# Performance work log

Measured on AMD Instinct MI355X. Metric: run time of the kernel, lower is better.

The kernel has to match this reference:

```python
import jax, jax.numpy as jnp
import numpy as np

B, N, C = 2, 2048, 768
H, HD = 12, 64
HID = 3072
LN_EPS = 1e-5
POL_EPS = 1e-6


def _layer_norm(x, g, b):
    m = jnp.mean(x, axis=-1, keepdims=True)
    v = jnp.mean(jnp.square(x - m), axis=-1, keepdims=True)
    return (x - m) * jax.lax.rsqrt(v + LN_EPS) * g + b


def _softmax_with_policy(attn, policy):
    # attn: [B,H,N,N], policy: [B,N,1]
    n = attn.shape[-1]
    ap = policy.reshape(policy.shape[0], 1, 1, n)  # [B,1,1,N]
    eye = jnp.eye(n, dtype=ap.dtype)[None, None]   # [1,1,N,N]
    ap = ap + (1.0 - ap) * eye                     # always attend to self
    attn = attn - jnp.max(attn, axis=-1, keepdims=True)
    attn = jnp.exp(attn.astype(jnp.float32)) * ap.astype(jnp.float32)
    attn = (attn + POL_EPS / n) / (jnp.sum(attn, axis=-1, keepdims=True) + POL_EPS)
    return attn


def setup_inputs() -> dict:
    key = jax.random.key(0)
    ks = jax.random.split(key, 12)
    s = lambda fan_in: 1.0 / np.sqrt(fan_in)
    x = jax.random.normal(ks[0], (B, N, C), dtype=jnp.float32)
    policy = (jax.random.uniform(ks[1], (B, N, 1)) > 0.5).astype(jnp.float32)
    return {
        "x": x,
        "policy": policy,
        "ln1_g": jnp.ones((C,), jnp.float32),
        "ln1_b": jnp.zeros((C,), jnp.float32),
        "qkv_w": jax.random.uniform(ks[2], (3 * H * HD, C), jnp.float32, -s(C), s(C)),
        "proj_w": jax.random.uniform(ks[3], (C, H * HD), jnp.float32, -s(H * HD), s(H * HD)),
        "proj_b": jnp.zeros((C,), jnp.float32),
        "ln2_g": jnp.ones((C,), jnp.float32),
        "ln2_b": jnp.zeros((C,), jnp.float32),
        "fc1_w": jax.random.uniform(ks[4], (HID, C), jnp.float32, -s(C), s(C)),
        "fc1_b": jnp.zeros((HID,), jnp.float32),
        "fc2_w": jax.random.uniform(ks[5], (C, HID), jnp.float32, -s(HID), s(HID)),
        "fc2_b": jnp.zeros((C,), jnp.float32),
    }


def reference(x, policy, ln1_g, ln1_b, qkv_w, proj_w, proj_b, ln2_g, ln2_b, fc1_w, fc1_b, fc2_w, fc2_b):
    b, n, c = x.shape
    scale = HD ** -0.5
    # --- attention branch (pre-LN) ---
    h = _layer_norm(x, ln1_g, ln1_b)
    qkv = (h @ qkv_w.T).reshape(b, n, 3, H, HD).transpose(2, 0, 3, 1, 4)  # [3,B,H,N,hd]
    q, k, v = qkv[0], qkv[1], qkv[2]
    attn = jnp.einsum("bhqd,bhkd->bhqk", q * scale, k)
    attn = _softmax_with_policy(attn, policy).astype(x.dtype)
    o = jnp.einsum("bhqk,bhkd->bhqd", attn, v).transpose(0, 2, 1, 3).reshape(b, n, H * HD)
    x = x + (o @ proj_w.T + proj_b)  # skip_lam = 1.0, dropout/drop_path = identity
    # --- MLP branch (pre-LN) ---
    h = _layer_norm(x, ln2_g, ln2_b)
    h = jax.nn.gelu(h @ fc1_w.T + fc1_b, approximate=False)  # torch nn.GELU = exact erf
    x = x + (h @ fc2_w.T + fc2_b)
    return x
```

## Files before the change

kernel.cpp:

```cpp
#include <hip/hip_runtime.h>

typedef unsigned short u16;
typedef unsigned int u32;
typedef float f32x4 __attribute__((ext_vector_type(4)));
typedef float f32x16 __attribute__((ext_vector_type(16)));
typedef __bf16 bf16x8 __attribute__((ext_vector_type(8)));
typedef u16 u16x4v __attribute__((ext_vector_type(4)));
typedef u32 u32x2 __attribute__((ext_vector_type(2)));
typedef u32 u32x4 __attribute__((ext_vector_type(4)));

#define NHEAD 12
#define NN 2048
#define CC 768

#define GLOBAL_AS __attribute__((address_space(1)))
#define LDS_AS __attribute__((address_space(3)))

__device__ __forceinline__ u16 tobf(float f) {
  __bf16 h = (__bf16)f;
  return __builtin_bit_cast(u16, h);
}
__device__ __forceinline__ float bf2f(u16 h) {
  u32 u = ((u32)h) << 16;
  return __builtin_bit_cast(float, u);
}
__device__ __forceinline__ u32 cvtpk(float lo, float hi) {
  u32 r;
  asm("v_cvt_pk_bf16_f32 %0, %1, %2" : "=v"(r) : "v"(lo), "v"(hi));
  return r;
}
__device__ __forceinline__ void plswap(u32& a, u32& b) {
  asm volatile("v_permlane32_swap_b32 %0, %1" : "+v"(a), "+v"(b));
}
__device__ __forceinline__ void plswapf(float& a, float& b) {
  asm volatile("v_permlane32_swap_b32 %0, %1" : "+v"(a), "+v"(b));
}
__device__ __forceinline__ float gelu_erf(float v) {
  float y = fabsf(v) * 0.70710678118654752f;
  float t = __builtin_amdgcn_rcpf(fmaf(0.3275911f, y, 1.f));
  float p = fmaf(1.061405429f, t, -1.453152027f);
  p = fmaf(p, t, 1.421413741f);
  p = fmaf(p, t, -0.284496736f);
  p = fmaf(p, t, 0.254829592f);
  p = p * t;
  float e = __builtin_amdgcn_exp2f(-y * y * 1.44269504f);
  float er = fmaf(-p, e, 1.f);
  er = (v < 0.f) ? -er : er;
  return 0.5f * v * (1.f + er);
}

#define N4_QKV 442368
#define N4_PROJ 147456
#define N4_FC 589824
__global__ __launch_bounds__(256) void cvt4_kernel(
    const float* __restrict__ a, const float* __restrict__ b,
    const float* __restrict__ c, const float* __restrict__ d,
    u16* __restrict__ oa, u16* __restrict__ ob, u16* __restrict__ oc,
    u16* __restrict__ od) {
  int i = blockIdx.x * 256 + threadIdx.x;
  const float* src;
  u16* dst;
  if (i < N4_QKV) {
    src = a; dst = oa;
  } else if (i < N4_QKV + N4_PROJ) {
    i -= N4_QKV; src = b; dst = ob;
  } else if (i < N4_QKV + N4_PROJ + N4_FC) {
    i -= N4_QKV + N4_PROJ; src = c; dst = oc;
  } else {
    i -= N4_QKV + N4_PROJ + N4_FC; src = d; dst = od;
    if (i >= N4_FC) return;
  }
  float4 v = ((const float4*)src)[i];
  u16x4v o = {tobf(v.x), tobf(v.y), tobf(v.z), tobf(v.w)};
  ((u16x4v*)dst)[i] = o;
}

__global__ __launch_bounds__(256) void ln_kernel(const float* __restrict__ x,
                                                 const float* __restrict__ gw,
                                                 const float* __restrict__ bw,
                                                 u16* __restrict__ out) {
  int row = blockIdx.x * 4 + (threadIdx.x >> 6);
  int lane = threadIdx.x & 63;
  const float* xr = x + (size_t)row * CC + lane * 12;
  float v[12];
  *(float4*)&v[0] = *(const float4*)(xr + 0);
  *(float4*)&v[4] = *(const float4*)(xr + 4);
  *(float4*)&v[8] = *(const float4*)(xr + 8);
  float s = 0.f, sq = 0.f;
#pragma unroll
  for (int j = 0; j < 12; ++j) { s += v[j]; sq += v[j] * v[j]; }
#pragma unroll
  for (int o = 1; o < 64; o <<= 1) { s += __shfl_xor(s, o); sq += __shfl_xor(sq, o); }
  float mean = s * (1.f / CC);
  float var = sq * (1.f / CC) - mean * mean;
  float rs = rsqrtf(var + 1e-5f);
  u16 ob[12];
#pragma unroll
  for (int j = 0; j < 12; ++j) {
    int c = lane * 12 + j;
    ob[j] = tobf((v[j] - mean) * rs * gw[c] + bw[c]);
  }
  u32* orow = (u32*)(out + (size_t)row * CC + lane * 12);
#pragma unroll
  for (int j = 0; j < 6; ++j) orow[j] = (u32)ob[2 * j] | ((u32)ob[2 * j + 1] << 16);
}

template <int BM, int BN, int OB, int HASB, int ACT, int RES>
__global__ __launch_bounds__(256) void gemm_kernel(
    const u16* __restrict__ A, const u16* __restrict__ Bw,
    const float* __restrict__ bias, const float* __restrict__ res,
    void* __restrict__ Cout, int M, int N, int K) {
  constexpr int MW = BM / 2;
  constexpr int MF = MW / 16;
  constexpr int NF = BN / 32;
  __shared__ __align__(16) u16 Alds[BM * 64];
  __shared__ __align__(16) u16 Blds[BN * 64];
  const int tid = threadIdx.x;
  const int lane = tid & 63, wave = tid >> 6;
  const int l15 = lane & 15, g = lane >> 4;
  const int nx = gridDim.x;
  const int flat = blockIdx.y * nx + blockIdx.x;
  const int cpx = (nx * gridDim.y) >> 3;
  const int swz = (flat & 7) * cpx + (flat >> 3);
  const int bm = (swz % nx) * BM, bn = (swz / nx) * BN;
  const int wm = (wave >> 1) * MW, wn = (wave & 1) * (BN / 2);
  f32x4 acc[MF][NF] = {};

  for (int kt = 0; kt < K; kt += 64) {
#pragma unroll
    for (int i = 0; i < BM / 32; ++i) {
      int ob_ = i * 4096 + wave * 1024;
      int lb = ob_ + lane * 16;
      int row = lb >> 7;
      int cb = (lb & 127) ^ ((row & 7) << 4);
      const u16* sa = A + (size_t)(bm + row) * K + kt + (cb >> 1);
      __builtin_amdgcn_global_load_lds((const GLOBAL_AS void*)sa,
                                       (LDS_AS void*)(Alds + (ob_ >> 1)), 16, 0, 0);
    }
#pragma unroll
    for (int i = 0; i < BN / 32; ++i) {
      int ob_ = i * 4096 + wave * 1024;
      int lb = ob_ + lane * 16;
      int row = lb >> 7;
      int cb = (lb & 127) ^ ((row & 7) << 4);
      const u16* sb = Bw + (size_t)(bn + row) * K + kt + (cb >> 1);
      __builtin_amdgcn_global_load_lds((const GLOBAL_AS void*)sb,
                                       (LDS_AS void*)(Blds + (ob_ >> 1)), 16, 0, 0);
    }
    __syncthreads();
#pragma unroll
    for (int ks = 0; ks < 2; ++ks) {
      bf16x8 af[MF], bfr[NF];
#pragma unroll
      for (int mi = 0; mi < MF; ++mi) {
        int row = wm + mi * 16 + l15;
        int cb = (ks * 64 + g * 16) ^ ((row & 7) << 4);
        af[mi] = *(const bf16x8*)&Alds[row * 64 + (cb >> 1)];
      }
#pragma unroll
      for (int ni = 0; ni < NF; ++ni) {
        int row = wn + ni * 16 + l15;
        int cb = (ks * 64 + g * 16) ^ ((row & 7) << 4);
        bfr[ni] = *(const bf16x8*)&Blds[row * 64 + (cb >> 1)];
      }
#pragma unroll
      for (int mi = 0; mi < MF; ++mi)
#pragma unroll
        for (int ni = 0; ni < NF; ++ni)
          acc[mi][ni] = __builtin_amdgcn_mfma_f32_16x16x32_bf16(af[mi], bfr[ni],
                                                                acc[mi][ni], 0, 0, 0);
    }
    __syncthreads();
  }
#pragma unroll
  for (int mi = 0; mi < MF; ++mi) {
#pragma unroll
    for (int ni = 0; ni < NF; ++ni) {
      int col = bn + wn + ni * 16 + l15;
      float bs = HASB ? bias[col] : 0.f;
#pragma unroll
      for (int r = 0; r < 4; ++r) {
        int rowm = bm + wm + mi * 16 + g * 4 + r;
        float v = acc[mi][ni][r] + bs;
        if (ACT) v = gelu_erf(v);
        if (RES) v += res[(size_t)rowm * N + col];
        if (OB)
          ((u16*)Cout)[(size_t)rowm * N + col] = tobf(v);
        else
          ((float*)Cout)[(size_t)rowm * N + col] = v;
      }
    }
  }
}

__global__ __launch_bounds__(256) void vsum_kernel(const u16* __restrict__ qkv,
                                                   float* __restrict__ vs) {
  int bh = blockIdx.x, q4 = blockIdx.y;
  int b = bh / NHEAD, h = bh % NHEAD;
  int d = threadIdx.x & 63, part = threadIdx.x >> 6;
  float s = 0.f;
  for (int n = q4 * 512 + part; n < q4 * 512 + 512; n += 4)
    s += bf2f(qkv[(size_t)(b * NN + n) * 2304 + 2 * CC + h * 64 + d]);
  __shared__ float red[256];
  red[threadIdx.x] = s;
  __syncthreads();
  if (threadIdx.x < 64) {
    float t = red[threadIdx.x] + red[threadIdx.x + 64] + red[threadIdx.x + 128] +
              red[threadIdx.x + 192];
    vs[q4 * (24 * 64) + bh * 64 + threadIdx.x] = t;
  }
}

__global__ __launch_bounds__(256) void scan_kernel(const float* __restrict__ policy,
                                                   int* __restrict__ ncbuf,
                                                   int* __restrict__ idxbuf) {
  int b = blockIdx.x, tid = threadIdx.x;
  float pv[8];
  *(float4*)&pv[0] = *(const float4*)&policy[b * NN + tid * 8];
  *(float4*)&pv[4] = *(const float4*)&policy[b * NN + tid * 8 + 4];
  int cnt = 0;
#pragma unroll
  for (int j = 0; j < 8; ++j) cnt += (pv[j] != 0.f) ? 1 : 0;
  __shared__ int sc[256];
  sc[tid] = cnt;
  __syncthreads();
  for (int off = 1; off < 256; off <<= 1) {
    int v = sc[tid];
    int add = (tid >= off) ? sc[tid - off] : 0;
    __syncthreads();
    sc[tid] = v + add;
    __syncthreads();
  }
  int base = sc[tid] - cnt;
#pragma unroll
  for (int j = 0; j < 8; ++j) {
    if (pv[j] != 0.f) idxbuf[b * NN + base++] = tid * 8 + j;
  }
  if (tid == 255) ncbuf[b] = sc[255];
}

__global__ __launch_bounds__(256) void gather_kernel(const u16* __restrict__ qkv,
                                                     const int* __restrict__ ncbuf,
                                                     const int* __restrict__ idxbuf,
                                                     u16* __restrict__ ckv) {
  int b = blockIdx.y;
  int nc = ncbuf[b];
  int ncp = (nc + 127) & ~127;
  int c = blockIdx.x * 256 + threadIdx.x;
  int j = c / 192, col = (c % 192) * 8;
  if (j >= ncp) return;
  uint4 val = {0, 0, 0, 0};
  if (j < nc) {
    int src = idxbuf[b * NN + j];
    val = *(const uint4*)&qkv[(size_t)(b * NN + src) * 2304 + CC + col];
  }
  *(uint4*)&ckv[(size_t)(b * NN + j) * 1536 + col] = val;
}

#define SCL2E 0.18033688f
#define TRRD(dst, addr, OFF) \
  asm volatile("ds_read_b64_tr_b16 %0, %1 offset:" OFF : "=v"(dst) : "v"(addr))

__global__ __launch_bounds__(256) void attn32_kernel(const u16* __restrict__ qkv,
                                                     const u16* __restrict__ ckv,
                                                     const int* __restrict__ ncbuf,
                                                     float* __restrict__ partO,
                                                     float* __restrict__ partlm) {
  __shared__ __align__(16) u16 Klds[2][4096];
  __shared__ __align__(16) u16 Vlds[2][4096];
  __shared__ float alf[4][32];
  const int bh = blockIdx.y, b = bh / NHEAD, h = bh % NHEAD;
  const int qt = blockIdx.x >> 1, half = blockIdx.x & 1;
  const int tid = threadIdx.x, lane = tid & 63, w = tid >> 6;
  const int l31 = lane & 31, hp = lane >> 5, b4 = (lane >> 4) & 1;
  const int q0 = qt * 128 + w * 32;
  const int nc = ncbuf[b];
  const int ncp = (nc + 127) & ~127;
  const int nh = ncp >> 1;
  const int nt = nh >> 6;
  const int kv0 = half * nh;
  const size_t adv = (size_t)64 * 1536;

  bf16x8 qf0, qf1, qf2, qf3;
  {
    const u16* qp = qkv + (size_t)(b * NN + q0 + l31) * 2304 + h * 64 + 8 * hp;
#pragma unroll
    for (int ds = 0; ds < 4; ++ds) {
      bf16x8 r = *(const bf16x8*)(qp + ds * 16);
      bf16x8 o;
#pragma unroll
      for (int j = 0; j < 8; ++j) o[j] = (__bf16)((float)r[j] * SCL2E);
      if (ds == 0) qf0 = o; else if (ds == 1) qf1 = o; else if (ds == 2) qf2 = o; else qf3 = o;
    }
  }

  const u16* ksrc[2];
  const u16* vsrcp[2];
#pragma unroll
  for (int c = 0; c < 2; ++c) {
    int lb = c * 4096 + w * 1024 + lane * 16;
    int row = lb >> 7;
    int cb = (lb & 127) ^ ((row & 7) << 4);
    ksrc[c] = ckv + (size_t)(b * NN + kv0 + row) * 1536 + h * 64 + (cb >> 1);
    int idx0 = (c * 256 + w * 64 + lane) * 8;
    int s0 = idx0 & 15, jj = (idx0 >> 4) & 3, b4v = (idx0 >> 6) & 1,
        pv = (idx0 >> 7) & 1, hv = (idx0 >> 8) & 1, dtv = (idx0 >> 9) & 1,
        mkv = (idx0 >> 10) & 3;
    int key = mkv * 16 + 8 * hv + 4 * pv + jj;
    int d0 = dtv * 32 + 16 * b4v + s0;
    vsrcp[c] = ckv + (size_t)(b * NN + kv0 + key) * 1536 + CC + h * 64 + d0;
  }
  auto stage = [&](int buf) {
#pragma unroll
    for (int c = 0; c < 2; ++c) {
      __builtin_amdgcn_global_load_lds((const GLOBAL_AS void*)ksrc[c],
                                       (LDS_AS void*)&Klds[buf][c * 2048 + w * 512], 16, 0, 0);
      __builtin_amdgcn_global_load_lds((const GLOBAL_AS void*)vsrcp[c],
                                       (LDS_AS void*)&Vlds[buf][c * 2048 + w * 512], 16, 0, 0);
      ksrc[c] += adv; vsrcp[c] += adv;
    }
  };

  stage(0);
  __syncthreads();

  float m_cur = -3.0e38f, m_true = -3.0e38f, l_run = 0.f;
  f32x16 accd[2] = {};
  const u32 vbase = (u32)(uintptr_t)(LDS_AS u16*)&Vlds[0][0] +
                    (u32)(2 * (lane & 15) + 128 * b4 + 512 * hp);

#pragma unroll 1
  for (int t = 0; t < nt; ++t) {
    const int cur = t & 1;
    if (t < nt - 1) stage(cur ^ 1);

    f32x16 sv0, sv1;
    {
      bf16x8 kf[4];
#pragma unroll
      for (int ds = 0; ds < 4; ++ds) {
        int row = l31;
        int cb = (32 * ds + 16 * hp) ^ ((row & 7) << 4);
        kf[ds] = *(const bf16x8*)((const char*)&Klds[cur][0] + row * 128 + cb);
      }
      f32x16 a = {};
      a = __builtin_amdgcn_mfma_f32_32x32x16_bf16(kf[0], qf0, a, 0, 0, 0);
      a = __builtin_amdgcn_mfma_f32_32x32x16_bf16(kf[1], qf1, a, 0, 0, 0);
      a = __builtin_amdgcn_mfma_f32_32x32x16_bf16(kf[2], qf2, a, 0, 0, 0);
      a = __builtin_amdgcn_mfma_f32_32x32x16_bf16(kf[3], qf3, a, 0, 0, 0);
      sv0 = a;
    }
    {
      bf16x8 kf[4];
#pragma unroll
      for (int ds = 0; ds < 4; ++ds) {
        int row = 32 + l31;
        int cb = (32 * ds + 16 * hp) ^ ((row & 7) << 4);
        kf[ds] = *(const bf16x8*)((const char*)&Klds[cur][0] + row * 128 + cb);
      }
      f32x16 a = {};
      a = __builtin_amdgcn_mfma_f32_32x32x16_bf16(kf[0], qf0, a, 0, 0, 0);
      a = __builtin_amdgcn_mfma_f32_32x32x16_bf16(kf[1], qf1, a, 0, 0, 0);
      a = __builtin_amdgcn_mfma_f32_32x32x16_bf16(kf[2], qf2, a, 0, 0, 0);
      a = __builtin_amdgcn_mfma_f32_32x32x16_bf16(kf[3], qf3, a, 0, 0, 0);
      sv1 = a;
    }

    u32x2 tr[4][2][2];
    {
      u32 vab = vbase + (u32)(cur * 8192);
      TRRD(tr[0][0][0], vab, "0");    TRRD(tr[0][0][1], vab, "256");
      TRRD(tr[0][1][0], vab, "1024"); TRRD(tr[0][1][1], vab, "1280");
      TRRD(tr[1][0][0], vab, "2048"); TRRD(tr[1][0][1], vab, "2304");
      TRRD(tr[1][1][0], vab, "3072"); TRRD(tr[1][1][1], vab, "3328");
      TRRD(tr[2][0][0], vab, "4096"); TRRD(tr[2][0][1], vab, "4352");
      TRRD(tr[3][0][0], vab, "6144"); TRRD(tr[3][0][1], vab, "6400");
      TRRD(tr[2][1][0], vab, "5120"); TRRD(tr[2][1][1], vab, "5376");
      TRRD(tr[3][1][0], vab, "7168"); TRRD(tr[3][1][1], vab, "7424");
    }

    float ta = fmaxf(fmaxf(sv0[0], sv0[1]), sv0[2]);
    float tb = fmaxf(fmaxf(sv0[3], sv0[4]), sv0[5]);
    float tc = fmaxf(fmaxf(sv0[6], sv0[7]), sv0[8]);
    float td = fmaxf(fmaxf(sv0[9], sv0[10]), sv0[11]);
    float te = fmaxf(fmaxf(sv0[12], sv0[13]), sv0[14]);
    float tf = fmaxf(fmaxf(sv0[15], sv1[0]), sv1[1]);
    float tg = fmaxf(fmaxf(sv1[2], sv1[3]), sv1[4]);
    float th = fmaxf(fmaxf(sv1[5], sv1[6]), sv1[7]);
    float ti = fmaxf(fmaxf(sv1[8], sv1[9]), sv1[10]);
    float tj = fmaxf(fmaxf(sv1[11], sv1[12]), sv1[13]);
    float tk = fmaxf(sv1[14], sv1[15]);
    float tmax = fmaxf(fmaxf(fmaxf(fmaxf(ta, tb), fmaxf(tc, td)),
                             fmaxf(fmaxf(te, tf), fmaxf(tg, th))),
                       fmaxf(fmaxf(ti, tj), tk));
    {
      float t1 = tmax, t2 = tmax;
      plswapf(t1, t2);
      tmax = fmaxf(t1, t2);
    }
    m_true = fmaxf(m_true, tmax);
    const bool defer = __all(tmax <= m_cur + 8.f);
    const float m_new = defer ? m_cur : fmaxf(m_cur, tmax);

    const int thr = nc - (kv0 + t * 64);
    float ev[32];
#pragma unroll
    for (int kt = 0; kt < 2; ++kt) {
#pragma unroll
      for (int i = 0; i < 4; ++i) {
#pragma unroll
        for (int rq = 0; rq < 4; ++rq) {
          int r = 4 * i + rq;
          int kidx = kt * 32 + 8 * i + 4 * hp + rq;
          float sval = kt ? sv1[r] : sv0[r];
          float e = __builtin_amdgcn_exp2f(sval - m_new);
          ev[kt * 16 + r] = (kidx < thr) ? e : 0.f;
        }
      }
    }
    u32 wv[16];
#pragma unroll
    for (int j = 0; j < 16; ++j) wv[j] = cvtpk(ev[2 * j], ev[2 * j + 1]);
    float ps[16];
#pragma unroll
    for (int j = 0; j < 16; ++j)
      ps[j] = __builtin_bit_cast(float, wv[j] << 16) +
              __builtin_bit_cast(float, wv[j] & 0xffff0000u);
#pragma unroll
    for (int s = 8; s > 0; s >>= 1)
#pragma unroll
      for (int j = 0; j < s; ++j) ps[j] += ps[j + s];
    float psum = ps[0];
    {
      float s1 = psum, s2 = psum;
      plswapf(s1, s2);
      psum = s1 + s2;
    }
    if (!defer) {
      float alpha = __builtin_amdgcn_exp2f(m_cur - m_new);
      l_run = l_run * alpha + psum;
      m_cur = m_new;
      if (lane < 32) alf[w][lane] = alpha;
      float4 aq0 = *(const float4*)&alf[w][4 * hp];
      float4 aq1 = *(const float4*)&alf[w][8 + 4 * hp];
      float4 aq2 = *(const float4*)&alf[w][16 + 4 * hp];
      float4 aq3 = *(const float4*)&alf[w][24 + 4 * hp];
#pragma unroll
      for (int dt = 0; dt < 2; ++dt) {
#pragma unroll
        for (int rq = 0; rq < 4; ++rq) {
          accd[dt][0 + rq] *= ((const float*)&aq0)[rq];
          accd[dt][4 + rq] *= ((const float*)&aq1)[rq];
          accd[dt][8 + rq] *= ((const float*)&aq2)[rq];
          accd[dt][12 + rq] *= ((const float*)&aq3)[rq];
        }
      }
    } else {
      l_run += psum;
    }

    u32 PK[4][4];
#pragma unroll
    for (int mk = 0; mk < 4; ++mk) {
      int bw_ = 8 * (mk >> 1) + 4 * (mk & 1);
      PK[mk][0] = wv[bw_ + 0];
      PK[mk][1] = wv[bw_ + 1];
      PK[mk][2] = wv[bw_ + 2];
      PK[mk][3] = wv[bw_ + 3];
      plswap(PK[mk][2], PK[mk][0]);
      plswap(PK[mk][3], PK[mk][1]);
    }

    asm volatile("s_waitcnt lgkmcnt(0)" ::: "memory");
    __builtin_amdgcn_sched_barrier(0);

#pragma unroll
    for (int mk = 0; mk < 4; ++mk) {
      u32x4 pk4 = {PK[mk][0], PK[mk][1], PK[mk][2], PK[mk][3]};
      bf16x8 pf = __builtin_bit_cast(bf16x8, pk4);
#pragma unroll
      for (int dt = 0; dt < 2; ++dt) {
        u32x4 vv = {tr[mk][dt][0].x, tr[mk][dt][0].y, tr[mk][dt][1].x, tr[mk][dt][1].y};
        bf16x8 vf = __builtin_bit_cast(bf16x8, vv);
        accd[dt] = __builtin_amdgcn_mfma_f32_32x32x16_bf16(pf, vf, accd[dt], 0, 0, 0);
      }
    }
    __syncthreads();
  }

  float sr = __builtin_amdgcn_exp2f(m_cur - m_true);
  if (lane < 32) {
    alf[w][lane] = sr;
    float2 lm = {l_run * sr, m_true};
    *(float2*)&partlm[2 * ((size_t)(half * 24 + bh) * 2048 + q0 + lane)] = lm;
  }
  float4 sq0 = *(const float4*)&alf[w][4 * hp];
  float4 sq1 = *(const float4*)&alf[w][8 + 4 * hp];
  float4 sq2 = *(const float4*)&alf[w][16 + 4 * hp];
  float4 sq3 = *(const float4*)&alf[w][24 + 4 * hp];
  float* pb2 = partO + ((size_t)(half * 24 + bh) * 2048) * 64;
#pragma unroll
  for (int dt = 0; dt < 2; ++dt) {
#pragma unroll
    for (int i = 0; i < 4; ++i) {
      float4 sqv = (i == 0) ? sq0 : (i == 1) ? sq1 : (i == 2) ? sq2 : sq3;
#pragma unroll
      for (int rq = 0; rq < 4; ++rq) {
        int row = q0 + 8 * i + 4 * hp + rq;
        pb2[(size_t)row * 64 + dt * 32 + l31] = accd[dt][4 * i + rq] * ((const float*)&sqv)[rq];
      }
    }
  }
}

__global__ __launch_bounds__(256) void merge_kernel(const float* __restrict__ partO,
                                                    const float* __restrict__ partlm,
                                                    const float* __restrict__ vs,
                                                    const float* __restrict__ policy,
                                                    const u16* __restrict__ qkv,
                                                    u16* __restrict__ o) {
  int rr = blockIdx.x * 4 + (threadIdx.x >> 6);
  int lane = threadIdx.x & 63;
  int bh = rr >> 11, q = rr & 2047;
  int b = bh / NHEAD, h = bh % NHEAD;
  const float* O1 = partO + ((size_t)bh * 2048 + q) * 64;
  const float* O2 = partO + ((size_t)(24 + bh) * 2048 + q) * 64;
  float2 lm1 = ((const float2*)partlm)[(size_t)bh * 2048 + q];
  float2 lm2 = ((const float2*)partlm)[(size_t)(24 + bh) * 2048 + q];
  float ms = fmaxf(lm1.y, lm2.y);
  float w1 = exp2f(lm1.y - ms), w2 = exp2f(lm2.y - ms);
  float num_d = 0.f, den_d = 0.f;
  if (policy[b * NN + q] == 0.f) {
    const u16* rowp = qkv + (size_t)(b * NN + q) * 2304 + h * 64 + lane;
    float qd = bf2f(rowp[0]);
    float kd = bf2f(rowp[CC]);
    float vv = bf2f(rowp[2 * CC]);
    float dp = qd * kd;
#pragma unroll
    for (int of = 1; of < 64; of <<= 1) dp += __shfl_xor(dp, of);
    float e = exp2f(dp * 0.18033688f - ms);
    num_d = e * vv;
    den_d = e;
  }
  float den = lm1.x * w1 + lm2.x * w2 + den_d + 1e-6f;
  float vsv = vs[bh * 64 + lane] + vs[1536 + bh * 64 + lane] +
              vs[3072 + bh * 64 + lane] + vs[4608 + bh * 64 + lane];
  float num = O1[lane] * w1 + O2[lane] * w2 + num_d + (1e-6f / 2048.f) * vsv;
  o[((size_t)(b * NN + q)) * CC + h * 64 + lane] = tobf(num / den);
}

extern "C" void kernel_launch(void* const* d_in, const int* in_sizes, int n_in,
                              void* d_out, int out_size, void* d_ws, size_t ws_size,
                              hipStream_t stream) {
  const float* x = (const float*)d_in[0];
  const float* policy = (const float*)d_in[1];
  const float* ln1g = (const float*)d_in[2];
  const float* ln1b = (const float*)d_in[3];
  const float* qkvw = (const float*)d_in[4];
  const float* projw = (const float*)d_in[5];
  const float* projb = (const float*)d_in[6];
  const float* ln2g = (const float*)d_in[7];
  const float* ln2b = (const float*)d_in[8];
  const float* fc1w = (const float*)d_in[9];
  const float* fc1b = (const float*)d_in[10];
  const float* fc2w = (const float*)d_in[11];
  const float* fc2b = (const float*)d_in[12];
  float* out = (float*)d_out;

  char* ws = (char*)d_ws;
  size_t off = 0;
  auto alloc = [&](size_t bytes) {
    void* p = ws + off;
    off = (off + bytes + 255) & ~(size_t)255;
    return p;
  };
  u16* wq = (u16*)alloc((size_t)2304 * 768 * 2);
  u16* wp = (u16*)alloc((size_t)768 * 768 * 2);
  u16* w1 = (u16*)alloc((size_t)3072 * 768 * 2);
  u16* w2 = (u16*)alloc((size_t)768 * 3072 * 2);
  u16* hbuf = (u16*)alloc((size_t)4096 * 768 * 2);
  u16* obuf = (u16*)alloc((size_t)4096 * 768 * 2);
  u16* qkv = (u16*)alloc((size_t)4096 * 2304 * 2);
  float* vs = (float*)alloc((size_t)4 * 24 * 64 * 4);
  int* ncbuf = (int*)alloc(2 * sizeof(int));
  int* idxbuf = (int*)alloc((size_t)2 * NN * sizeof(int));
  size_t unionOff = off;
  float* partO = (float*)alloc((size_t)2 * 24 * 2048 * 64 * 4);
  float* partlm = (float*)alloc((size_t)2 * 24 * 2048 * 2 * 4);
  float* x1 = (float*)(ws + unionOff);
  u16* ckv = hbuf;
  u16* f1 = obuf;

  cvt4_kernel<<<6912, 256, 0, stream>>>(qkvw, projw, fc1w, fc2w, wq, wp, w1, w2);

  ln_kernel<<<1024, 256, 0, stream>>>(x, ln1g, ln1b, hbuf);
  gemm_kernel<64, 128, 1, 0, 0, 0><<<dim3(64, 18), 256, 0, stream>>>(
      hbuf, wq, nullptr, nullptr, qkv, 4096, 2304, 768);
  vsum_kernel<<<dim3(24, 4), 256, 0, stream>>>(qkv, vs);
  scan_kernel<<<2, 256, 0, stream>>>(policy, ncbuf, idxbuf);
  gather_kernel<<<dim3(1536, 2), 256, 0, stream>>>(qkv, ncbuf, idxbuf, ckv);
  attn32_kernel<<<dim3(32, 24), 256, 0, stream>>>(qkv, ckv, ncbuf, partO, partlm);
  merge_kernel<<<12288, 256, 0, stream>>>(partO, partlm, vs, policy, qkv, obuf);
  gemm_kernel<64, 64, 0, 1, 0, 1><<<dim3(64, 12), 256, 0, stream>>>(
      obuf, wp, projb, x, x1, 4096, 768, 768);
  ln_kernel<<<1024, 256, 0, stream>>>(x1, ln2g, ln2b, hbuf);
  gemm_kernel<64, 128, 1, 1, 1, 0><<<dim3(64, 24), 256, 0, stream>>>(
      hbuf, w1, fc1b, nullptr, f1, 4096, 3072, 768);
  gemm_kernel<64, 64, 0, 1, 0, 1><<<dim3(64, 12), 256, 0, stream>>>(
      f1, w2, fc2b, x1, out, 4096, 768, 3072);
}
```

Baseline: 222.2 us.

## Fuse attention merge into kernel, drop KV split for full-range blocks

```diff
diff --git a/kernel.cpp b/kernel.cpp
--- a/kernel.cpp
+++ b/kernel.cpp
@@ -261,24 +261,23 @@
 #define TRRD(dst, addr, OFF) \
   asm volatile("ds_read_b64_tr_b16 %0, %1 offset:" OFF : "=v"(dst) : "v"(addr))
 
-__global__ __launch_bounds__(256) void attn32_kernel(const u16* __restrict__ qkv,
+__global__ __launch_bounds__(128) void attn32_kernel(const u16* __restrict__ qkv,
                                                      const u16* __restrict__ ckv,
                                                      const int* __restrict__ ncbuf,
-                                                     float* __restrict__ partO,
-                                                     float* __restrict__ partlm) {
+                                                     const float* __restrict__ policy,
+                                                     const float* __restrict__ vsum,
+                                                     u16* __restrict__ o) {
   __shared__ __align__(16) u16 Klds[2][4096];
   __shared__ __align__(16) u16 Vlds[2][4096];
-  __shared__ float alf[4][32];
+  __shared__ float alf[2][32];
+  __shared__ float4 alfe[2][32];
   const int bh = blockIdx.y, b = bh / NHEAD, h = bh % NHEAD;
-  const int qt = blockIdx.x >> 1, half = blockIdx.x & 1;
   const int tid = threadIdx.x, lane = tid & 63, w = tid >> 6;
   const int l31 = lane & 31, hp = lane >> 5, b4 = (lane >> 4) & 1;
-  const int q0 = qt * 128 + w * 32;
+  const int q0 = blockIdx.x * 64 + w * 32;
   const int nc = ncbuf[b];
   const int ncp = (nc + 127) & ~127;
-  const int nh = ncp >> 1;
-  const int nt = nh >> 6;
-  const int kv0 = half * nh;
+  const int nt = ncp >> 6;
   const size_t adv = (size_t)64 * 1536;
 
   bf16x8 qf0, qf1, qf2, qf3;
@@ -287,36 +286,37 @@
 #pragma unroll
     for (int ds = 0; ds < 4; ++ds) {
       bf16x8 r = *(const bf16x8*)(qp + ds * 16);
-      bf16x8 o;
-#pragma unroll
-      for (int j = 0; j < 8; ++j) o[j] = (__bf16)((float)r[j] * SCL2E);
-      if (ds == 0) qf0 = o; else if (ds == 1) qf1 = o; else if (ds == 2) qf2 = o; else qf3 = o;
-    }
-  }
-
-  const u16* ksrc[2];
-  const u16* vsrcp[2];
-#pragma unroll
-  for (int c = 0; c < 2; ++c) {
-    int lb = c * 4096 + w * 1024 + lane * 16;
+      bf16x8 oo;
+#pragma unroll
+      for (int j = 0; j < 8; ++j) oo[j] = (__bf16)((float)r[j] * SCL2E);
+      if (ds == 0) qf0 = oo; else if (ds == 1) qf1 = oo; else if (ds == 2) qf2 = oo; else qf3 = oo;
+    }
+  }
+
+  const u16* ksrc[4];
+  const u16* vsrcp[4];
+#pragma unroll
+  for (int c = 0; c < 4; ++c) {
+    int L = c * 128 + w * 64 + lane;
+    int lb = L * 16;
     int row = lb >> 7;
     int cb = (lb & 127) ^ ((row & 7) << 4);
-    ksrc[c] = ckv + (size_t)(b * NN + kv0 + row) * 1536 + h * 64 + (cb >> 1);
-    int idx0 = (c * 256 + w * 64 + lane) * 8;
+    ksrc[c] = ckv + (size_t)(b * NN + row) * 1536 + h * 64 + (cb >> 1);
+    int idx0 = L * 8;
     int s0 = idx0 & 15, jj = (idx0 >> 4) & 3, b4v = (idx0 >> 6) & 1,
         pv = (idx0 >> 7) & 1, hv = (idx0 >> 8) & 1, dtv = (idx0 >> 9) & 1,
         mkv = (idx0 >> 10) & 3;
     int key = mkv * 16 + 8 * hv + 4 * pv + jj;
     int d0 = dtv * 32 + 16 * b4v + s0;
-    vsrcp[c] = ckv + (size_t)(b * NN + kv0 + key) * 1536 + CC + h * 64 + d0;
+    vsrcp[c] = ckv + (size_t)(b * NN + key) * 1536 + CC + h * 64 + d0;
   }
   auto stage = [&](int buf) {
 #pragma unroll
-    for (int c = 0; c < 2; ++c) {
+    for (int c = 0; c < 4; ++c) {
       __builtin_amdgcn_global_load_lds((const GLOBAL_AS void*)ksrc[c],
-                                       (LDS_AS void*)&Klds[buf][c * 2048 + w * 512], 16, 0, 0);
+                                       (LDS_AS void*)&Klds[buf][c * 1024 + w * 512], 16, 0, 0);
       __builtin_amdgcn_global_load_lds((const GLOBAL_AS void*)vsrcp[c],
-                                       (LDS_AS void*)&Vlds[buf][c * 2048 + w * 512], 16, 0, 0);
+                                       (LDS_AS void*)&Vlds[buf][c * 1024 + w * 512], 16, 0, 0);
       ksrc[c] += adv; vsrcp[c] += adv;
     }
   };
@@ -402,7 +402,7 @@
     const bool defer = __all(tmax <= m_cur + 8.f);
     const float m_new = defer ? m_cur : fmaxf(m_cur, tmax);
 
-    const int thr = nc - (kv0 + t * 64);
+    const int thr = nc - t * 64;
     float ev[32];
 #pragma unroll
     for (int kt = 0; kt < 2; ++kt) {
@@ -489,64 +489,50 @@
   }
 
   float sr = __builtin_amdgcn_exp2f(m_cur - m_true);
+  float dp;
+  {
+    const u16* kp = qkv + (size_t)(b * NN + q0 + l31) * 2304 + CC + h * 64 + 8 * hp;
+    float acc_dp = 0.f;
+#pragma unroll
+    for (int ds = 0; ds < 4; ++ds) {
+      bf16x8 kr = *(const bf16x8*)(kp + ds * 16);
+      const bf16x8& qv = (ds == 0) ? qf0 : (ds == 1) ? qf1 : (ds == 2) ? qf2 : qf3;
+#pragma unroll
+      for (int j = 0; j < 8; ++j) acc_dp += (float)qv[j] * (float)kr[j];
+    }
+    float d2 = acc_dp;
+    plswapf(acc_dp, d2);
+    dp = acc_dp + d2;
+  }
+  float pol = policy[b * NN + q0 + l31];
+  float ed = (pol == 0.f) ? __builtin_amdgcn_exp2f(dp - m_true) : 0.f;
   if (lane < 32) {
-    alf[w][lane] = sr;
-    float2 lm = {l_run * sr, m_true};
-    *(float2*)&partlm[2 * ((size_t)(half * 24 + bh) * 2048 + q0 + lane)] = lm;
-  }
-  float4 sq0 = *(const float4*)&alf[w][4 * hp];
-  float4 sq1 = *(const float4*)&alf[w][8 + 4 * hp];
-  float4 sq2 = *(const float4*)&alf[w][16 + 4 * hp];
-  float4 sq3 = *(const float4*)&alf[w][24 + 4 * hp];
-  float* pb2 = partO + ((size_t)(half * 24 + bh) * 2048) * 64;
-#pragma unroll
-  for (int dt = 0; dt < 2; ++dt) {
-#pragma unroll
-    for (int i = 0; i < 4; ++i) {
-      float4 sqv = (i == 0) ? sq0 : (i == 1) ? sq1 : (i == 2) ? sq2 : sq3;
-#pragma unroll
-      for (int rq = 0; rq < 4; ++rq) {
-        int row = q0 + 8 * i + 4 * hp + rq;
-        pb2[(size_t)row * 64 + dt * 32 + l31] = accd[dt][4 * i + rq] * ((const float*)&sqv)[rq];
-      }
-    }
-  }
-}
-
-__global__ __launch_bounds__(256) void merge_kernel(const float* __restrict__ partO,
-                                                    const float* __restrict__ partlm,
-                                                    const float* __restrict__ vs,
-                                                    const float* __restrict__ policy,
-                                                    const u16* __restrict__ qkv,
-                                                    u16* __restrict__ o) {
-  int rr = blockIdx.x * 4 + (threadIdx.x >> 6);
-  int lane = threadIdx.x & 63;
-  int bh = rr >> 11, q = rr & 2047;
-  int b = bh / NHEAD, h = bh % NHEAD;
-  const float* O1 = partO + ((size_t)bh * 2048 + q) * 64;
-  const float* O2 = partO + ((size_t)(24 + bh) * 2048 + q) * 64;
-  float2 lm1 = ((const float2*)partlm)[(size_t)bh * 2048 + q];
-  float2 lm2 = ((const float2*)partlm)[(size_t)(24 + bh) * 2048 + q];
-  float ms = fmaxf(lm1.y, lm2.y);
-  float w1 = exp2f(lm1.y - ms), w2 = exp2f(lm2.y - ms);
-  float num_d = 0.f, den_d = 0.f;
-  if (policy[b * NN + q] == 0.f) {
-    const u16* rowp = qkv + (size_t)(b * NN + q) * 2304 + h * 64 + lane;
-    float qd = bf2f(rowp[0]);
-    float kd = bf2f(rowp[CC]);
-    float vv = bf2f(rowp[2 * CC]);
-    float dp = qd * kd;
-#pragma unroll
-    for (int of = 1; of < 64; of <<= 1) dp += __shfl_xor(dp, of);
-    float e = exp2f(dp * 0.18033688f - ms);
-    num_d = e * vv;
-    den_d = e;
-  }
-  float den = lm1.x * w1 + lm2.x * w2 + den_d + 1e-6f;
-  float vsv = vs[bh * 64 + lane] + vs[1536 + bh * 64 + lane] +
-              vs[3072 + bh * 64 + lane] + vs[4608 + bh * 64 + lane];
-  float num = O1[lane] * w1 + O2[lane] * w2 + num_d + (1e-6f / 2048.f) * vsv;
-  o[((size_t)(b * NN + q)) * CC + h * 64 + lane] = tobf(num / den);
+    float4 pk = {l_run * sr, ed, sr, 0.f};
+    alfe[w][lane] = pk;
+  }
+  float vsv0 = vsum[bh * 64 + l31] + vsum[1536 + bh * 64 + l31] +
+               vsum[3072 + bh * 64 + l31] + vsum[4608 + bh * 64 + l31];
+  float vsv1 = vsum[bh * 64 + 32 + l31] + vsum[1536 + bh * 64 + 32 + l31] +
+               vsum[3072 + bh * 64 + 32 + l31] + vsum[4608 + bh * 64 + 32 + l31];
+  const float epsn = 1e-6f / (float)NN;
+#pragma unroll
+  for (int i = 0; i < 4; ++i) {
+#pragma unroll
+    for (int rq = 0; rq < 4; ++rq) {
+      int r = 8 * i + 4 * hp + rq;
+      float4 brd = alfe[w][r];
+      const u16* vrow = qkv + (size_t)(b * NN + q0 + r) * 2304 + 2 * CC + h * 64;
+      float den = brd.x + brd.y + 1e-6f;
+      float rden = __builtin_amdgcn_rcpf(den);
+#pragma unroll
+      for (int dt = 0; dt < 2; ++dt) {
+        float vval = bf2f(vrow[dt * 32 + l31]);
+        float vsv = dt ? vsv1 : vsv0;
+        float num = accd[dt][4 * i + rq] * brd.z + brd.y * vval + epsn * vsv;
+        o[(size_t)(b * NN + q0 + r) * CC + h * 64 + dt * 32 + l31] = tobf(num * rden);
+      }
+    }
+  }
 }
 
 extern "C" void kernel_launch(void* const* d_in, const int* in_sizes, int n_in,
@@ -584,11 +570,8 @@
   float* vs = (float*)alloc((size_t)4 * 24 * 64 * 4);
   int* ncbuf = (int*)alloc(2 * sizeof(int));
   int* idxbuf = (int*)alloc((size_t)2 * NN * sizeof(int));
-  size_t unionOff = off;
-  float* partO = (float*)alloc((size_t)2 * 24 * 2048 * 64 * 4);
-  float* partlm = (float*)alloc((size_t)2 * 24 * 2048 * 2 * 4);
-  float* x1 = (float*)(ws + unionOff);
-  u16* ckv = hbuf;
+  u16* ckv = (u16*)alloc((size_t)2 * NN * 1536 * 2);
+  float* x1 = (float*)alloc((size_t)4096 * 768 * 4);
   u16* f1 = obuf;
 
   cvt4_kernel<<<6912, 256, 0, stream>>>(qkvw, projw, fc1w, fc2w, wq, wp, w1, w2);
@@ -599,8 +582,7 @@
   vsum_kernel<<<dim3(24, 4), 256, 0, stream>>>(qkv, vs);
   scan_kernel<<<2, 256, 0, stream>>>(policy, ncbuf, idxbuf);
   gather_kernel<<<dim3(1536, 2), 256, 0, stream>>>(qkv, ncbuf, idxbuf, ckv);
-  attn32_kernel<<<dim3(32, 24), 256, 0, stream>>>(qkv, ckv, ncbuf, partO, partlm);
-  merge_kernel<<<12288, 256, 0, stream>>>(partO, partlm, vs, policy, qkv, obuf);
+  attn32_kernel<<<dim3(32, 24), 128, 0, stream>>>(qkv, ckv, ncbuf, policy, vs, obuf);
   gemm_kernel<64, 64, 0, 1, 0, 1><<<dim3(64, 12), 256, 0, stream>>>(
       obuf, wp, projb, x, x1, 4096, 768, 768);
   ln_kernel<<<1024, 256, 0, stream>>>(x1, ln2g, ln2b, hbuf);
```

After: 214.5 us (median of 2 runs). 1.04x faster.
